# Performance work log

Hardware: AMD Instinct MI355X
Metric: run time of the kernel (lower is better)

The kernel has to match this reference:

```python
import jax, jax.numpy as jnp
import numpy as np

B, G, D = 16, 20000, 64   # batch, num_genes, feature_dim
S, L = 500, 128           # num_gene_sets, max genes per set (padded)


def setup_inputs() -> dict:
    key = jax.random.key(0)
    k1, k2, k3 = jax.random.split(key, 3)
    gene_features = jax.random.normal(k1, (B, G, D), dtype=jnp.float32)
    geneset_indices = jax.random.randint(k2, (S, L), 0, G, dtype=jnp.int32)
    set_mask = jnp.ones((S, L), dtype=bool)  # all positions valid (uniform-size sets)
    attn_weights = jax.random.normal(k3, (S, L, D), dtype=jnp.float32)
    return {
        "gene_features": gene_features,
        "attn_weights": attn_weights,
        "geneset_indices": geneset_indices,
        "set_mask": set_mask,
    }


def reference(gene_features, attn_weights, geneset_indices, set_mask):
    # Gather per-set gene features: [B, S, L, D]
    gathered = jnp.take(gene_features, geneset_indices, axis=1)
    # Masked softmax over the set-member axis L (independent per feature dim),
    # matching F.softmax(attention_weights, dim=1) per gene set.
    neg = jnp.finfo(attn_weights.dtype).min
    logits = jnp.where(set_mask[:, :, None], attn_weights, neg)  # [S, L, D]
    attn = jax.nn.softmax(logits, axis=1)                        # [S, L, D]
    # Weighted sum over set members -> [B, S, D]
    return jnp.einsum('bsld,sld->bsd', gathered, attn)
```

## Files before the change

### kernel.cpp

```cpp
#include <hip/hip_runtime.h>
#include <math.h>


#define NB 16
#define NG 20000
#define ND 64
#define NS 500
#define NL 128

typedef unsigned short ushortx8 __attribute__((ext_vector_type(8)));
typedef float floatx8 __attribute__((ext_vector_type(8)));

__device__ __forceinline__ float bf2f(unsigned short u) {
    union { unsigned int i; float f; } x;
    x.i = ((unsigned int)u) << 16;
    return x.f;
}

__device__ __forceinline__ unsigned short f2bf(float f) {
    union { float f; unsigned int i; } x;
    x.f = f;
    unsigned int r = x.i + 0x7FFFu + ((x.i >> 16) & 1u);
    return (unsigned short)(r >> 16);
}

__global__ void detect_dtype_kernel(const unsigned short* __restrict__ aw,
                                    int* __restrict__ flag) {
    const unsigned int e = ((unsigned int)aw[2 * threadIdx.x] >> 7) & 0xFFu;
    const unsigned long long m = __ballot(e >= 100u && e <= 135u);
    if (threadIdx.x == 0) *flag = (__popcll(m) >= 32) ? 1 : 0;
}

template<bool BF16>
__global__ __launch_bounds__(1024)
void agg_kernel(const void* __restrict__ gf_,
                const void* __restrict__ aw_,
                const int*  __restrict__ idx,
                void*       __restrict__ out_,
                const int*  __restrict__ flag)
{
    if (*flag != (BF16 ? 1 : 0)) return;

    __shared__ float attn_s[NL * ND];
    __shared__ float red[16 * ND];
    __shared__ float inv_sum[ND];
    __shared__ int   gidx[NL];
    __shared__ float part_red[8 * 16 * 8 * 10];

    const int s = blockIdx.x;
    const int t = threadIdx.x;

    if (t < NL) gidx[t] = idx[s * NL + t];

    const int d    = t & 63;
    const int part = t >> 6;
    const unsigned short* awp = (const unsigned short*)aw_ + (size_t)s * (NL * ND);

    float m = -INFINITY;
    #pragma unroll
    for (int i = 0; i < 8; ++i) {
        const int l = part * 8 + i;
        const float v = BF16 ? bf2f(awp[l * ND + d])
                             : ((const float*)aw_)[(size_t)s * (NL * ND) + l * ND + d];
        attn_s[l * ND + d] = v;
        m = fmaxf(m, v);
    }
    red[part * ND + d] = m;
    __syncthreads();

    const int q  = t & 7;
    const int bl = (t >> 3) & 15;
    const int lp = t >> 7;
    const int d0 = q * 8;

    int goff[16];
    #pragma unroll
    for (int k = 0; k < 16; ++k) {
        const int g = __builtin_amdgcn_readfirstlane(gidx[lp * 16 + k]);
        goff[k] = g * (BF16 ? (ND * 2) : (ND * 4));
    }

    float m_all = -INFINITY;
    #pragma unroll
    for (int p = 0; p < 16; ++p) m_all = fmaxf(m_all, red[p * ND + d]);
    __syncthreads();

    float psum = 0.f;
    #pragma unroll
    for (int i = 0; i < 8; ++i) {
        const int l = part * 8 + i;
        const float e = __expf(attn_s[l * ND + d] - m_all);
        attn_s[l * ND + d] = e;
        psum += e;
    }
    red[part * ND + d] = psum;
    __syncthreads();
    if (part == 0) {
        float tot = 0.f;
        #pragma unroll
        for (int p = 0; p < 16; ++p) tot += red[p * ND + d];
        inv_sum[d] = 1.0f / tot;
    }
    __syncthreads();

    float acc[8];
    #pragma unroll
    for (int j = 0; j < 8; ++j) acc[j] = 0.f;

    if (BF16) {
        const char* gbase = (const char*)gf_ + (size_t)bl * (NG * ND * 2) + d0 * 2;
        #pragma unroll
        for (int k = 0; k < 16; ++k) {
            const int l = lp * 16 + k;
            const ushortx8 u = *(const ushortx8*)(gbase + goff[k]);
            const floatx8  w = *(const floatx8*)&attn_s[l * ND + d0];
            #pragma unroll
            for (int j = 0; j < 8; ++j) acc[j] += bf2f(u[j]) * w[j];
        }
    } else {
        const char* gbase = (const char*)gf_ + (size_t)bl * (NG * ND * 4) + d0 * 4;
        #pragma unroll
        for (int k = 0; k < 16; ++k) {
            const int l = lp * 16 + k;
            const floatx8 u = *(const floatx8*)(gbase + goff[k]);
            const floatx8 w = *(const floatx8*)&attn_s[l * ND + d0];
            #pragma unroll
            for (int j = 0; j < 8; ++j) acc[j] += u[j] * w[j];
        }
    }

    float* pr = &part_red[((lp * 16 + bl) * 8 + q) * 10];
    #pragma unroll
    for (int j = 0; j < 8; j += 2)
        *(float2*)&pr[j] = make_float2(acc[j], acc[j + 1]);
    __syncthreads();

    const int bl2 = t >> 6;
    const int dd  = t & 63;
    const int qq  = dd >> 3;
    const int jj  = dd & 7;
    float r = 0.f;
    #pragma unroll
    for (int p = 0; p < 8; ++p)
        r += part_red[((p * 16 + bl2) * 8 + qq) * 10 + jj];
    r *= inv_sum[dd];
    if (BF16)
        ((unsigned short*)out_)[((size_t)bl2 * NS + s) * ND + dd] = f2bf(r);
    else
        ((float*)out_)[((size_t)bl2 * NS + s) * ND + dd] = r;
}

extern "C" void kernel_launch(void* const* d_in, const int* in_sizes, int n_in,
                              void* d_out, int out_size, void* d_ws, size_t ws_size,
                              hipStream_t stream) {
    const void* gf  = d_in[0];
    const void* aw  = d_in[1];
    const int*  idx = (const int*)d_in[2];
    int* flag = (int*)d_ws;

    detect_dtype_kernel<<<1, 64, 0, stream>>>((const unsigned short*)aw, flag);
    agg_kernel<true ><<<NS, 1024, 0, stream>>>(gf, aw, idx, d_out, flag);
    agg_kernel<false><<<NS, 1024, 0, stream>>>(gf, aw, idx, d_out, flag);
}
```

Measured before the change: 158.6 us.

## Map one wave per batch and reduce partial sums with lane shuffles

Reassigns threads so each 64-lane wave handles one batch row, with lanes split across 8 L-partitions and 8 feature chunks. The cross-partition reduction now uses __shfl_xor within the wave instead of a shared-memory buffer, a barrier and a second reduction pass, and the output is written as 8-wide vector stores. Gene indices are read from LDS inside the loop, which is only partially unrolled, replacing the precomputed scalar readfirstlane offsets. Each wave now gathers from 8 different rows per load instead of one uniform row per lane group, which may change the memory access pattern and raise VGPR address cost.

```diff
diff --git a/kernel.cpp b/kernel.cpp
--- a/kernel.cpp
+++ b/kernel.cpp
@@ -45,7 +45,6 @@
     __shared__ float red[16 * ND];
     __shared__ float inv_sum[ND];
     __shared__ int   gidx[NL];
-    __shared__ float part_red[8 * 16 * 8 * 10];
 
     const int s = blockIdx.x;
     const int t = threadIdx.x;
@@ -67,19 +66,6 @@
     }
     red[part * ND + d] = m;
     __syncthreads();
-
-    const int q  = t & 7;
-    const int bl = (t >> 3) & 15;
-    const int lp = t >> 7;
-    const int d0 = q * 8;
-
-    int goff[16];
-    #pragma unroll
-    for (int k = 0; k < 16; ++k) {
-        const int g = __builtin_amdgcn_readfirstlane(gidx[lp * 16 + k]);
-        goff[k] = g * (BF16 ? (ND * 2) : (ND * 4));
-    }
-
     float m_all = -INFINITY;
     #pragma unroll
     for (int p = 0; p < 16; ++p) m_all = fmaxf(m_all, red[p * ND + d]);
@@ -103,51 +89,61 @@
     }
     __syncthreads();
 
+    const int b    = t >> 6;
+    const int lane = t & 63;
+    const int lp   = lane >> 3;
+    const int q    = lane & 7;
+    const int d0   = q * 8;
+
     float acc[8];
     #pragma unroll
     for (int j = 0; j < 8; ++j) acc[j] = 0.f;
 
     if (BF16) {
-        const char* gbase = (const char*)gf_ + (size_t)bl * (NG * ND * 2) + d0 * 2;
-        #pragma unroll
+        const char* gbase = (const char*)gf_ + (size_t)b * (NG * ND * 2) + d0 * 2;
+        #pragma unroll 4
         for (int k = 0; k < 16; ++k) {
             const int l = lp * 16 + k;
-            const ushortx8 u = *(const ushortx8*)(gbase + goff[k]);
+            const int g = gidx[l];
+            const ushortx8 u = *(const ushortx8*)(gbase + (size_t)g * (ND * 2));
             const floatx8  w = *(const floatx8*)&attn_s[l * ND + d0];
             #pragma unroll
             for (int j = 0; j < 8; ++j) acc[j] += bf2f(u[j]) * w[j];
         }
     } else {
-        const char* gbase = (const char*)gf_ + (size_t)bl * (NG * ND * 4) + d0 * 4;
-        #pragma unroll
+        const char* gbase = (const char*)gf_ + (size_t)b * (NG * ND * 4) + d0 * 4;
+        #pragma unroll 4
         for (int k = 0; k < 16; ++k) {
             const int l = lp * 16 + k;
-            const floatx8 u = *(const floatx8*)(gbase + goff[k]);
+            const int g = gidx[l];
+            const floatx8 u = *(const floatx8*)(gbase + (size_t)g * (ND * 4));
             const floatx8 w = *(const floatx8*)&attn_s[l * ND + d0];
             #pragma unroll
             for (int j = 0; j < 8; ++j) acc[j] += u[j] * w[j];
         }
     }
 
-    float* pr = &part_red[((lp * 16 + bl) * 8 + q) * 10];
     #pragma unroll
-    for (int j = 0; j < 8; j += 2)
-        *(float2*)&pr[j] = make_float2(acc[j], acc[j + 1]);
-    __syncthreads();
+    for (int j = 0; j < 8; ++j) {
+        acc[j] += __shfl_xor(acc[j], 8);
+        acc[j] += __shfl_xor(acc[j], 16);
+        acc[j] += __shfl_xor(acc[j], 32);
+    }
 
-    const int bl2 = t >> 6;
-    const int dd  = t & 63;
-    const int qq  = dd >> 3;
-    const int jj  = dd & 7;
-    float r = 0.f;
-    #pragma unroll
-    for (int p = 0; p < 8; ++p)
-        r += part_red[((p * 16 + bl2) * 8 + qq) * 10 + jj];
-    r *= inv_sum[dd];
-    if (BF16)
-        ((unsigned short*)out_)[((size_t)bl2 * NS + s) * ND + dd] = f2bf(r);
-    else
-        ((float*)out_)[((size_t)bl2 * NS + s) * ND + dd] = r;
+    if (lp == 0) {
+        const floatx8 inv = *(const floatx8*)&inv_sum[d0];
+        if (BF16) {
+            ushortx8 o;
+            #pragma unroll
+            for (int j = 0; j < 8; ++j) o[j] = f2bf(acc[j] * inv[j]);
+            *(ushortx8*)((unsigned short*)out_ + ((size_t)b * NS + s) * ND + d0) = o;
+        } else {
+            floatx8 o;
+            #pragma unroll
+            for (int j = 0; j < 8; ++j) o[j] = acc[j] * inv[j];
+            *(floatx8*)((float*)out_ + ((size_t)b * NS + s) * ND + d0) = o;
+        }
+    }
 }
 
 extern "C" void kernel_launch(void* const* d_in, const int* in_sizes, int n_in,
```

After: 150.7 us. 1.05x faster.
